# Kernel tuning notes

Hardware: AMD Instinct MI355X
Metric: run time of the kernel (lower is better)

Reference implementation:

```python
import jax, jax.numpy as jnp
import numpy as np

LEVELS = 8
DB2 = [0.4829629131445341, 0.8365163037378079, 0.22414386804185735, -0.12940952255092145]


def make_wavelet(h):
    # g = flip(h); g[1::2] *= -1  (torch compute_wavelet)
    g = jnp.flip(h, -1)
    sign = jnp.where(jnp.arange(g.shape[-1]) % 2 == 0, 1.0, -1.0).astype(g.dtype)
    return g * sign


def circ_conv(x, f, tr=False):
    # FFT-based circular convolution, output length == input length (NORM='backward').
    L = x.shape[-1]
    F = jnp.fft.rfft(f, n=L)
    if tr:
        F = jnp.conj(F)  # circular correlation for the synthesis side
    return jnp.fft.irfft(jnp.fft.rfft(x, n=L) * F, n=L)


def despawn_forward(x, scaling):
    levels = scaling.shape[0]
    L = x.shape[1]
    D = 2 ** int(np.ceil(np.log2(L)))
    pl = (D - L) // 2
    pr = int(np.ceil((D - L) / 2))
    x = jnp.pad(x, ((0, 0), (pl, pr)), mode='edge')  # ReplicationPad1d

    # Analysis: per-level circular filter + dyadic downsample
    approx = x
    details_list = []
    for lev in range(levels):
        h = scaling[lev]
        g = make_wavelet(h)
        d = circ_conv(approx, g)[:, ::2]
        approx = circ_conv(approx, h)[:, ::2]
        details_list.append(d)
    coeffs = details_list + [approx]

    # Synthesis: zero-insert upsample + circular correlation (no thresholding,
    # matching the original forward which never applies HardThreshold)
    rec = approx
    for lev in reversed(range(levels)):
        h = scaling[lev]
        g = make_wavelet(h)
        d = details_list[lev]
        n, m = d.shape
        ud = jnp.zeros((n, 2 * m), d.dtype).at[:, ::2].set(d)
        ua = jnp.zeros((n, 2 * m), rec.dtype).at[:, ::2].set(rec)
        rec = circ_conv(ud, g, tr=True) + circ_conv(ua, h, tr=True)

    return rec[:, pl:L + pr], jnp.concatenate(coeffs, axis=-1)


def setup_inputs() -> dict:
    key = jax.random.key(0)
    k1, _ = jax.random.split(key)
    x = jax.random.normal(k1, (2048, 8192), dtype=jnp.float32)
    scaling = jnp.tile(jnp.asarray(DB2, dtype=jnp.float32), (LEVELS, 1))  # (levels, 4)
    return {"x": x, "scaling": scaling}


def reference(x, scaling):
    return despawn_forward(x, scaling)
```

## Files before the change

### kernel.cpp

```cpp
#include <hip/hip_runtime.h>

#define COLS   8192
#define LEVELS 8
#define TPB    512

__global__ __launch_bounds__(TPB) void despawn_kernel(
    const float* __restrict__ x, const float* __restrict__ scaling,
    float* __restrict__ out, int rows)
{
    __shared__ __align__(16) float B[COLS / 2];
    __shared__ __align__(16) float C[COLS / 4];
    __shared__ float filt[LEVELS * 4];

    const int row = blockIdx.x;
    const int tid = threadIdx.x;

    if (tid < LEVELS * 4) filt[tid] = scaling[tid];
    __syncthreads();

    const float* __restrict__ xg       = x + (size_t)row * COLS;
    float* __restrict__       out_rec  = out + (size_t)row * COLS;
    float* __restrict__       out_coef = out + (size_t)rows * COLS + (size_t)row * COLS;

    {
        const float h0 = filt[0], h1 = filt[1], h2 = filt[2], h3 = filt[3];
        const float g0 = h3, g1 = -h2, g2 = h1, g3 = -h0;
        const float4* __restrict__ xg4 = reinterpret_cast<const float4*>(xg);
        const int q = COLS / 4, qm = q - 1;
        for (int i = tid; i < q; i += TPB) {
            const float4 vb = xg4[i];
            const float4 va = xg4[(i - 1) & qm];
            const float d0 = g0*vb.x + g1*va.w + g2*va.z + g3*va.y;
            const float a0 = h0*vb.x + h1*va.w + h2*va.z + h3*va.y;
            const float d1 = g0*vb.z + g1*vb.y + g2*vb.x + g3*va.w;
            const float a1 = h0*vb.z + h1*vb.y + h2*vb.x + h3*va.w;
            reinterpret_cast<float2*>(out_coef)[i] = make_float2(d0, d1);
            reinterpret_cast<float2*>(B)[i]        = make_float2(a0, a1);
        }
        __syncthreads();
    }

    int n = COLS / 2, coff = COLS / 2;
    float* cur = B;
    float* nxt = C;
    for (int lev = 1; lev < LEVELS; ++lev) {
        const float h0 = filt[4*lev+0], h1 = filt[4*lev+1],
                    h2 = filt[4*lev+2], h3 = filt[4*lev+3];
        const float g0 = h3, g1 = -h2, g2 = h1, g3 = -h0;
        const int half = n >> 1;
        const int hq = half >> 1, hm = hq - 1;
        const bool lastlev = (lev == LEVELS - 1);
        const float4* c4 = reinterpret_cast<const float4*>(cur);
        for (int p = tid; p < hq; p += TPB) {
            const float4 vb = c4[p];
            const float4 va = c4[(p - 1) & hm];
            const float d0 = g0*vb.x + g1*va.w + g2*va.z + g3*va.y;
            const float a0 = h0*vb.x + h1*va.w + h2*va.z + h3*va.y;
            const float d1 = g0*vb.z + g1*vb.y + g2*vb.x + g3*va.w;
            const float a1 = h0*vb.z + h1*vb.y + h2*vb.x + h3*va.w;
            reinterpret_cast<float2*>(out_coef + coff)[p] = make_float2(d0, d1);
            reinterpret_cast<float2*>(nxt)[p]             = make_float2(a0, a1);
            if (lastlev)
                reinterpret_cast<float2*>(out_coef + coff + half)[p] = make_float2(a0, a1);
        }
        __syncthreads();
        coff += half;
        n = half;
        float* t = cur; cur = nxt; nxt = t;
    }

    int m = COLS >> LEVELS;
    const float* aprev = cur;
    int doff = COLS - 2 * m;
    for (int lev = LEVELS - 1; lev >= 0; --lev) {
        const float h0 = filt[4*lev+0], h1 = filt[4*lev+1],
                    h2 = filt[4*lev+2], h3 = filt[4*lev+3];
        const float g0 = h3, g1 = -h2, g2 = h1, g3 = -h0;
        const float2* __restrict__ d2 = reinterpret_cast<const float2*>(out_coef + doff);
        const float2* a2 = reinterpret_cast<const float2*>(aprev);
        const int mp = m >> 1, mm = mp - 1;
        float* rec = (lev & 1) ? B : C;
        const bool last = (lev == 0);
        for (int p = tid; p < mp; p += TPB) {
            const float2 dv0 = d2[p];
            const float2 dv1 = d2[(p + 1) & mm];
            const float2 av0 = a2[p];
            const float2 av1 = a2[(p + 1) & mm];
            const float r0 = g0*dv0.x + g2*dv0.y + h0*av0.x + h2*av0.y;
            const float r1 = g1*dv0.y + g3*dv1.x + h1*av0.y + h3*av1.x;
            const float r2 = g0*dv0.y + g2*dv1.x + h0*av0.y + h2*av1.x;
            const float r3 = g1*dv1.x + g3*dv1.y + h1*av1.x + h3*av1.y;
            if (last)
                reinterpret_cast<float4*>(out_rec)[p] = make_float4(r0, r1, r2, r3);
            else
                reinterpret_cast<float4*>(rec)[p]     = make_float4(r0, r1, r2, r3);
        }
        __syncthreads();
        aprev = rec;
        m <<= 1;
        doff -= m;
    }
}

extern "C" void kernel_launch(void* const* d_in, const int* in_sizes, int n_in,
                              void* d_out, int out_size, void* d_ws, size_t ws_size,
                              hipStream_t stream) {
    const float* x       = (const float*)d_in[0];
    const float* scaling = (const float*)d_in[1];
    float* out           = (float*)d_out;
    const int rows = in_sizes[0] / COLS;
    despawn_kernel<<<rows, TPB, 0, stream>>>(x, scaling, out, rows);
}
```

Baseline: 44.80 us.

## Run small wavelet levels in one wavefront and keep mid details in LDS

Levels 4-7 of both the analysis and the synthesis now run inside a single 64-thread wavefront using wave barriers instead of block-wide __syncthreads. The goal is to remove the many block-level barriers spent on tiny levels. Detail coefficients for levels 2-7 are also kept in a new LDS buffer, so synthesis reads them from shared memory rather than re-reading them from global. The analysis loops now emit float4 stores per thread, and the final barrier is skipped. The trade-offs are more LDS per block, which may lower occupancy, and serialized work on one wave while the other waves sit idle.

```diff
diff --git a/kernel.cpp b/kernel.cpp
--- a/kernel.cpp
+++ b/kernel.cpp
@@ -10,6 +10,7 @@
 {
     __shared__ __align__(16) float B[COLS / 2];
     __shared__ __align__(16) float C[COLS / 4];
+    __shared__ __align__(16) float D[COLS / 4];
     __shared__ float filt[LEVELS * 4];
 
     const int row = blockIdx.x;
@@ -26,80 +27,150 @@
         const float h0 = filt[0], h1 = filt[1], h2 = filt[2], h3 = filt[3];
         const float g0 = h3, g1 = -h2, g2 = h1, g3 = -h0;
         const float4* __restrict__ xg4 = reinterpret_cast<const float4*>(xg);
-        const int q = COLS / 4, qm = q - 1;
-        for (int i = tid; i < q; i += TPB) {
-            const float4 vb = xg4[i];
-            const float4 va = xg4[(i - 1) & qm];
-            const float d0 = g0*vb.x + g1*va.w + g2*va.z + g3*va.y;
-            const float a0 = h0*vb.x + h1*va.w + h2*va.z + h3*va.y;
-            const float d1 = g0*vb.z + g1*vb.y + g2*vb.x + g3*va.w;
-            const float a1 = h0*vb.z + h1*vb.y + h2*vb.x + h3*va.w;
-            reinterpret_cast<float2*>(out_coef)[i] = make_float2(d0, d1);
-            reinterpret_cast<float2*>(B)[i]        = make_float2(a0, a1);
+        const int q8 = COLS / 8, qm = COLS / 4 - 1;
+        for (int i = tid; i < q8; i += TPB) {
+            const float4 va = xg4[(2 * i - 1) & qm];
+            const float4 vb = xg4[2 * i];
+            const float4 vc = xg4[2 * i + 1];
+            float4 dv, av;
+            dv.x = g0*vb.x + g1*va.w + g2*va.z + g3*va.y;
+            av.x = h0*vb.x + h1*va.w + h2*va.z + h3*va.y;
+            dv.y = g0*vb.z + g1*vb.y + g2*vb.x + g3*va.w;
+            av.y = h0*vb.z + h1*vb.y + h2*vb.x + h3*va.w;
+            dv.z = g0*vc.x + g1*vb.w + g2*vb.z + g3*vb.y;
+            av.z = h0*vc.x + h1*vb.w + h2*vb.z + h3*vb.y;
+            dv.w = g0*vc.z + g1*vc.y + g2*vc.x + g3*vb.w;
+            av.w = h0*vc.z + h1*vc.y + h2*vc.x + h3*vb.w;
+            reinterpret_cast<float4*>(out_coef)[i] = dv;
+            reinterpret_cast<float4*>(B)[i]        = av;
         }
         __syncthreads();
     }
 
-    int n = COLS / 2, coff = COLS / 2;
+    int n = COLS / 2, coff = COLS / 2, dOff = 0;
     float* cur = B;
     float* nxt = C;
-    for (int lev = 1; lev < LEVELS; ++lev) {
+    for (int lev = 1; lev <= 3; ++lev) {
         const float h0 = filt[4*lev+0], h1 = filt[4*lev+1],
                     h2 = filt[4*lev+2], h3 = filt[4*lev+3];
         const float g0 = h3, g1 = -h2, g2 = h1, g3 = -h0;
-        const int half = n >> 1;
-        const int hq = half >> 1, hm = hq - 1;
-        const bool lastlev = (lev == LEVELS - 1);
+        const int half = n >> 1, qq = half >> 2, qm = (n >> 2) - 1;
         const float4* c4 = reinterpret_cast<const float4*>(cur);
-        for (int p = tid; p < hq; p += TPB) {
-            const float4 vb = c4[p];
-            const float4 va = c4[(p - 1) & hm];
-            const float d0 = g0*vb.x + g1*va.w + g2*va.z + g3*va.y;
-            const float a0 = h0*vb.x + h1*va.w + h2*va.z + h3*va.y;
-            const float d1 = g0*vb.z + g1*vb.y + g2*vb.x + g3*va.w;
-            const float a1 = h0*vb.z + h1*vb.y + h2*vb.x + h3*va.w;
-            reinterpret_cast<float2*>(out_coef + coff)[p] = make_float2(d0, d1);
-            reinterpret_cast<float2*>(nxt)[p]             = make_float2(a0, a1);
-            if (lastlev)
-                reinterpret_cast<float2*>(out_coef + coff + half)[p] = make_float2(a0, a1);
+        float4* o4 = reinterpret_cast<float4*>(out_coef + coff);
+        float4* n4 = reinterpret_cast<float4*>(nxt);
+        float4* D4 = reinterpret_cast<float4*>(D + dOff);
+        const bool toD = (lev >= 2);
+        for (int p = tid; p < qq; p += TPB) {
+            const float4 va = c4[(2 * p - 1) & qm];
+            const float4 vb = c4[2 * p];
+            const float4 vc = c4[2 * p + 1];
+            float4 dv, av;
+            dv.x = g0*vb.x + g1*va.w + g2*va.z + g3*va.y;
+            av.x = h0*vb.x + h1*va.w + h2*va.z + h3*va.y;
+            dv.y = g0*vb.z + g1*vb.y + g2*vb.x + g3*va.w;
+            av.y = h0*vb.z + h1*vb.y + h2*vb.x + h3*va.w;
+            dv.z = g0*vc.x + g1*vb.w + g2*vb.z + g3*vb.y;
+            av.z = h0*vc.x + h1*vb.w + h2*vb.z + h3*vb.y;
+            dv.w = g0*vc.z + g1*vc.y + g2*vc.x + g3*vb.w;
+            av.w = h0*vc.z + h1*vc.y + h2*vc.x + h3*vb.w;
+            o4[p] = dv;
+            n4[p] = av;
+            if (toD) D4[p] = dv;
         }
         __syncthreads();
         coff += half;
+        if (toD) dOff += half;
         n = half;
         float* t = cur; cur = nxt; nxt = t;
     }
 
-    int m = COLS >> LEVELS;
-    const float* aprev = cur;
-    int doff = COLS - 2 * m;
-    for (int lev = LEVELS - 1; lev >= 0; --lev) {
+    if (tid < 64) {
+        float* acur = C;
+        float* anxt = B;
+        int nn = 512, coffW = 7680, dW = 1536;
+        for (int lev = 4; lev <= 7; ++lev) {
+            const float h0 = filt[4*lev+0], h1 = filt[4*lev+1],
+                        h2 = filt[4*lev+2], h3 = filt[4*lev+3];
+            const float g0 = h3, g1 = -h2, g2 = h1, g3 = -h0;
+            const int half = nn >> 1, mask = nn - 1;
+            for (int i = tid; i < half; i += 64) {
+                const int b = 2 * i;
+                const float x0 = acur[b];
+                const float x1 = acur[(b - 1) & mask];
+                const float x2 = acur[(b - 2) & mask];
+                const float x3 = acur[(b - 3) & mask];
+                const float d = g0*x0 + g1*x1 + g2*x2 + g3*x3;
+                const float a = h0*x0 + h1*x1 + h2*x2 + h3*x3;
+                D[dW + i] = d;
+                out_coef[coffW + i] = d;
+                if (lev == 7) { D[2016 + i] = a; out_coef[8160 + i] = a; }
+                else          anxt[i] = a;
+            }
+            __builtin_amdgcn_wave_barrier();
+            coffW += half; dW += half; nn = half;
+            float* t = acur; acur = anxt; anxt = t;
+        }
+        int mS = 32, dS = 1984;
+        const float* aprevW = D + 2016;
+        for (int lev = 7; lev >= 4; --lev) {
+            const float h0 = filt[4*lev+0], h1 = filt[4*lev+1],
+                        h2 = filt[4*lev+2], h3 = filt[4*lev+3];
+            const float g0 = h3, g1 = -h2, g2 = h1, g3 = -h0;
+            const int mm = mS - 1;
+            float* recW = (lev & 1) ? B : C;
+            for (int j = tid; j < mS; j += 64) {
+                const float dj  = D[dS + j];
+                const float dj1 = D[dS + ((j + 1) & mm)];
+                const float dj2 = D[dS + ((j + 2) & mm)];
+                const float aj  = aprevW[j];
+                const float aj1 = aprevW[(j + 1) & mm];
+                const float aj2 = aprevW[(j + 2) & mm];
+                recW[2*j]     = g0*dj  + g2*dj1 + h0*aj  + h2*aj1;
+                recW[2*j + 1] = g1*dj1 + g3*dj2 + h1*aj1 + h3*aj2;
+            }
+            __builtin_amdgcn_wave_barrier();
+            aprevW = recW; mS <<= 1; dS -= mS;
+        }
+    }
+    __syncthreads();
+
+#define SYNTH_BODY(d2)                                                        \
+    for (int p = tid; p < mp; p += TPB) {                                     \
+        const float2 dv0 = (d2)[p];                                           \
+        const float2 dv1 = (d2)[(p + 1) & mm];                                \
+        const float2 av0 = a2[p];                                             \
+        const float2 av1 = a2[(p + 1) & mm];                                  \
+        const float r0 = g0*dv0.x + g2*dv0.y + h0*av0.x + h2*av0.y;           \
+        const float r1 = g1*dv0.y + g3*dv1.x + h1*av0.y + h3*av1.x;           \
+        const float r2 = g0*dv0.y + g2*dv1.x + h0*av0.y + h2*av1.x;           \
+        const float r3 = g1*dv1.x + g3*dv1.y + h1*av1.x + h3*av1.y;           \
+        const float4 rv = make_float4(r0, r1, r2, r3);                        \
+        if (last) reinterpret_cast<float4*>(out_rec)[p] = rv;                 \
+        else      reinterpret_cast<float4*>(rec)[p]     = rv;                 \
+    }
+
+    const float* aprev = C;
+    int m = 512;
+    for (int lev = 3; lev >= 0; --lev) {
         const float h0 = filt[4*lev+0], h1 = filt[4*lev+1],
                     h2 = filt[4*lev+2], h3 = filt[4*lev+3];
         const float g0 = h3, g1 = -h2, g2 = h1, g3 = -h0;
-        const float2* __restrict__ d2 = reinterpret_cast<const float2*>(out_coef + doff);
+        const int mp = m >> 1, mm = mp - 1;
         const float2* a2 = reinterpret_cast<const float2*>(aprev);
-        const int mp = m >> 1, mm = mp - 1;
         float* rec = (lev & 1) ? B : C;
         const bool last = (lev == 0);
-        for (int p = tid; p < mp; p += TPB) {
-            const float2 dv0 = d2[p];
-            const float2 dv1 = d2[(p + 1) & mm];
-            const float2 av0 = a2[p];
-            const float2 av1 = a2[(p + 1) & mm];
-            const float r0 = g0*dv0.x + g2*dv0.y + h0*av0.x + h2*av0.y;
-            const float r1 = g1*dv0.y + g3*dv1.x + h1*av0.y + h3*av1.x;
-            const float r2 = g0*dv0.y + g2*dv1.x + h0*av0.y + h2*av1.x;
-            const float r3 = g1*dv1.x + g3*dv1.y + h1*av1.x + h3*av1.y;
-            if (last)
-                reinterpret_cast<float4*>(out_rec)[p] = make_float4(r0, r1, r2, r3);
-            else
-                reinterpret_cast<float4*>(rec)[p]     = make_float4(r0, r1, r2, r3);
+        if (lev >= 2) {
+            const float2* dL = reinterpret_cast<const float2*>(D + ((lev == 3) ? 1024 : 0));
+            SYNTH_BODY(dL)
+        } else {
+            const float2* __restrict__ dG =
+                reinterpret_cast<const float2*>(out_coef + ((lev == 1) ? 4096 : 0));
+            SYNTH_BODY(dG)
         }
-        __syncthreads();
-        aprev = rec;
-        m <<= 1;
-        doff -= m;
+        if (lev) __syncthreads();
+        aprev = rec; m <<= 1;
     }
+#undef SYNTH_BODY
 }
 
 extern "C" void kernel_launch(void* const* d_in, const int* in_sizes, int n_in,
```

After: 42.80 us. 1.05x faster.
